# Optimization experiments

Measured on AMD Instinct MI355X. Metric: run time of the kernel, lower is better.

The kernel has to match this reference:

```python
import jax, jax.numpy as jnp
import numpy as np

D_MODEL = 1024
N_HEADS = 16
HEAD_DIM = D_MODEL // N_HEADS
D_FF = 4096
B, T = 2, 2048


def layernorm(x, g, b, eps=1e-5):
    mu = jnp.mean(x, axis=-1, keepdims=True)
    var = jnp.var(x, axis=-1, keepdims=True)
    return (x - mu) * jax.lax.rsqrt(var + eps) * g + b


def setup_inputs() -> dict:
    key = jax.random.key(0)
    ks = jax.random.split(key, 8)
    s = 0.02
    return {
        "x": jax.random.normal(ks[0], (B, T, D_MODEL), dtype=jnp.float32),
        "ln1_g": jnp.ones((D_MODEL,), jnp.float32),
        "ln1_b": jnp.zeros((D_MODEL,), jnp.float32),
        "qkv_w": jax.random.normal(ks[1], (D_MODEL, 3 * D_MODEL), jnp.float32) * s,
        "qkv_b": jnp.zeros((3 * D_MODEL,), jnp.float32),
        "proj_w": jax.random.normal(ks[2], (D_MODEL, D_MODEL), jnp.float32) * s,
        "proj_b": jnp.zeros((D_MODEL,), jnp.float32),
        "ln2_g": jnp.ones((D_MODEL,), jnp.float32),
        "ln2_b": jnp.zeros((D_MODEL,), jnp.float32),
        "mlp_w1": jax.random.normal(ks[3], (D_MODEL, D_FF), jnp.float32) * s,
        "mlp_b1": jnp.zeros((D_FF,), jnp.float32),
        "mlp_w2": jax.random.normal(ks[4], (D_FF, D_MODEL), jnp.float32) * s,
        "mlp_b2": jnp.zeros((D_MODEL,), jnp.float32),
    }


def reference(x, ln1_g, ln1_b, qkv_w, qkv_b, proj_w, proj_b,
              ln2_g, ln2_b, mlp_w1, mlp_b1, mlp_w2, mlp_b2):
    Bv, Tv, C = x.shape
    scale = HEAD_DIM ** -0.5
    # --- attention branch ---
    h = layernorm(x, ln1_g, ln1_b)
    qkv = h @ qkv_w + qkv_b                                   # [B,T,3C]
    qkv = qkv.reshape(Bv, Tv, 3, N_HEADS, HEAD_DIM)
    q, k, v = qkv[:, :, 0], qkv[:, :, 1], qkv[:, :, 2]        # [B,T,H,Dh]
    att = jnp.einsum('bqhd,bkhd->bhqk', q, k) * scale         # [B,H,T,T]
    causal = jnp.tril(jnp.ones((Tv, Tv), dtype=bool))
    att = jnp.where(causal[None, None], att, -jnp.inf)
    att = jax.nn.softmax(att, axis=-1)
    out = jnp.einsum('bhqk,bkhd->bqhd', att, v).reshape(Bv, Tv, C)
    out = out @ proj_w + proj_b
    x = x + out
    # --- mlp branch ---
    h2 = layernorm(x, ln2_g, ln2_b)
    h2 = jax.nn.gelu(h2 @ mlp_w1 + mlp_b1, approximate=False)
    x = x + (h2 @ mlp_w2 + mlp_b2)
    return x
```

## Files before the change

kernel.cpp:

```cpp
#include <hip/hip_runtime.h>
#include <hip/hip_bf16.h>
#include <cstdint>

typedef __attribute__((ext_vector_type(4))) float f32x4;
typedef __attribute__((ext_vector_type(16))) float f32x16;
typedef __attribute__((ext_vector_type(8))) __bf16 bf16x8;
typedef __attribute__((ext_vector_type(4))) __bf16 bf16x4;
typedef __attribute__((ext_vector_type(4))) uint32_t u32x4;
typedef __attribute__((ext_vector_type(2))) unsigned int u32x2;

#define EPI_BF16 0
#define EPI_GELU 1
#define EPI_RES  2

__device__ __forceinline__ void gll16(const void* g, void* l) {
  __builtin_amdgcn_global_load_lds((__attribute__((address_space(1))) void*)(g),
                                   (__attribute__((address_space(3))) void*)(l), 16, 0, 0);
}

__global__ __launch_bounds__(256)
void convT(const float* __restrict__ W, __bf16* __restrict__ WT, int Kd, int Nd)
{
  __shared__ __bf16 t[64][72];
  const int tid = threadIdx.x;
  const int n0 = blockIdx.x * 64, k0 = blockIdx.y * 64;
#pragma unroll
  for (int i = 0; i < 4; ++i) {
    const int c = i * 256 + tid;
    const int r = c >> 4, cc = (c & 15) * 4;
    const float4 v = *(const float4*)(W + (size_t)(k0 + r) * Nd + n0 + cc);
    bf16x4 tv; tv[0] = (__bf16)v.x; tv[1] = (__bf16)v.y; tv[2] = (__bf16)v.z; tv[3] = (__bf16)v.w;
    *(bf16x4*)&t[r][cc] = tv;
  }
  __syncthreads();
#pragma unroll
  for (int i = 0; i < 2; ++i) {
    const int c = i * 256 + tid;
    const int n = c >> 3, s = (c & 7) * 8;
    bf16x8 o;
#pragma unroll
    for (int j = 0; j < 8; ++j) o[j] = t[s + j][n];
    *(bf16x8*)(WT + (size_t)(n0 + n) * Kd + k0 + s) = o;
  }
}

__global__ __launch_bounds__(256)
void ln_rows(const float* __restrict__ x, const float* __restrict__ g,
             const float* __restrict__ b, __bf16* __restrict__ out)
{
  const int row = blockIdx.x;
  const int tid = threadIdx.x;
  const float4 v = *(const float4*)(x + (size_t)row * 1024 + tid * 4);
  float s = v.x + v.y + v.z + v.w;
  float q = v.x * v.x + v.y * v.y + v.z * v.z + v.w * v.w;
#pragma unroll
  for (int o = 32; o; o >>= 1) { s += __shfl_xor(s, o); q += __shfl_xor(q, o); }
  __shared__ float red[8];
  const int wid = tid >> 6;
  if ((tid & 63) == 0) { red[wid] = s; red[4 + wid] = q; }
  __syncthreads();
  s = red[0] + red[1] + red[2] + red[3];
  q = red[4] + red[5] + red[6] + red[7];
  const float mu = s * (1.0f / 1024.0f);
  const float var = q * (1.0f / 1024.0f) - mu * mu;
  const float rs = rsqrtf(var + 1e-5f);
  bf16x4 o4;
#pragma unroll
  for (int i = 0; i < 4; ++i) {
    const int c = tid * 4 + i;
    const float xv = (&v.x)[i];
    o4[i] = (__bf16)((xv - mu) * rs * g[c] + b[c]);
  }
  *(bf16x4*)(out + (size_t)row * 1024 + tid * 4) = o4;
}

template<int EPI>
__global__ __launch_bounds__(256)
void gemm_bt(const __bf16* __restrict__ A, const __bf16* __restrict__ BT,
             const float* __restrict__ bias, const float* __restrict__ R,
             void* __restrict__ Out, int M, int N, int K)
{
  const int tid = threadIdx.x;
  const int lane = tid & 63, wid = tid >> 6;
  const int l15 = lane & 15, lg = lane >> 4;
  const int wm = (wid >> 1) * 64, wn = (wid & 1) * 64;
  const int rowBase = blockIdx.y * 128, colBase = blockIdx.x * 128;
  __shared__ __bf16 As[128 * 32];
  __shared__ __bf16 Bs[128 * 32];
  f32x4 acc[4][4] = {};

  for (int k0 = 0; k0 < K; k0 += 32) {
#pragma unroll
    for (int i = 0; i < 2; ++i) {
      const int c = i * 256 + tid;
      const int r = c >> 2, s = (c & 3) * 8;
      gll16(A + (size_t)(rowBase + r) * K + (k0 + s), As + c * 8);
    }
#pragma unroll
    for (int i = 0; i < 2; ++i) {
      const int c = i * 256 + tid;
      const int r = c >> 2, s = (c & 3) * 8;
      gll16(BT + (size_t)(colBase + r) * K + (k0 + s), Bs + c * 8);
    }
    __syncthreads();
    bf16x8 af[4], bfr[4];
#pragma unroll
    for (int m = 0; m < 4; ++m) af[m] = *(const bf16x8*)(As + (wm + m * 16 + l15) * 32 + lg * 8);
#pragma unroll
    for (int n = 0; n < 4; ++n) bfr[n] = *(const bf16x8*)(Bs + (wn + n * 16 + l15) * 32 + lg * 8);
#pragma unroll
    for (int m = 0; m < 4; ++m)
#pragma unroll
      for (int n = 0; n < 4; ++n)
        acc[m][n] = __builtin_amdgcn_mfma_f32_16x16x32_bf16(af[m], bfr[n], acc[m][n], 0, 0, 0);
    __syncthreads();
  }
#pragma unroll
  for (int m = 0; m < 4; ++m) {
#pragma unroll
    for (int n = 0; n < 4; ++n) {
      const int col = colBase + wn + n * 16 + l15;
      const float bb = bias[col];
#pragma unroll
      for (int i = 0; i < 4; ++i) {
        const int row = rowBase + wm + m * 16 + lg * 4 + i;
        float v = acc[m][n][i] + bb;
        if constexpr (EPI == EPI_GELU) {
          v = 0.5f * v * (1.0f + erff(v * 0.70710678118654752f));
          ((__bf16*)Out)[(size_t)row * N + col] = (__bf16)v;
        } else if constexpr (EPI == EPI_BF16) {
          ((__bf16*)Out)[(size_t)row * N + col] = (__bf16)v;
        } else {
          v += R[(size_t)row * N + col];
          ((float*)Out)[(size_t)row * N + col] = v;
        }
      }
    }
  }
}

__global__ __launch_bounds__(256)
void rearrange(const __bf16* __restrict__ qkv, __bf16* __restrict__ Q,
               __bf16* __restrict__ Kb, __bf16* __restrict__ VT)
{
  __shared__ __bf16 vt[64][72];
  const int tid = threadIdx.x;
  const int bid = blockIdx.x;
  const int bh = bid >> 5, tt = bid & 31;
  const int b = bh >> 4, h = bh & 15;
  const int t0 = tt * 64;
#pragma unroll
  for (int i = 0; i < 2; ++i) {
    const int c = i * 256 + tid;
    const int tk = c >> 3, d0 = (c & 7) * 8;
    const size_t srow = (size_t)(b * 2048 + t0 + tk) * 3072 + h * 64 + d0;
    const size_t drow = (size_t)(bh * 2048 + t0 + tk) * 64 + d0;
    *(bf16x8*)(Q + drow) = *(const bf16x8*)(qkv + srow);
    *(bf16x8*)(Kb + drow) = *(const bf16x8*)(qkv + srow + 1024);
    *(bf16x8*)&vt[tk][d0] = *(const bf16x8*)(qkv + srow + 2048);
  }
  __syncthreads();
#pragma unroll
  for (int i = 0; i < 2; ++i) {
    const int c = i * 256 + tid;
    const int d = c >> 3, s = (c & 7) * 8;
    bf16x8 o;
#pragma unroll
    for (int j = 0; j < 8; ++j) o[j] = vt[s + j][d];
    *(bf16x8*)(VT + (size_t)(bh * 64 + d) * 2048 + t0 + s) = o;
  }
}

__global__ __launch_bounds__(128)
void attn(const __bf16* __restrict__ Q, const __bf16* __restrict__ K,
          const __bf16* __restrict__ VT, __bf16* __restrict__ O)
{
  const int bid = blockIdx.x;
  const int bh = bid >> 5, qt = 31 - (bid & 31);
  const int tid = threadIdx.x;
  const int lane = tid & 63, w = tid >> 6;
  const int l31 = lane & 31, hi = lane >> 5;
  __shared__ __bf16 Ks[64 * 64];
  __shared__ __bf16 Vs[64 * 64];
  const size_t base = (size_t)bh * 2048 * 64;
  const int qrow0 = qt * 64 + w * 32;
  const int xsw = (l31 & 7) << 3;

  bf16x8 qf[4];
#pragma unroll
  for (int s = 0; s < 4; ++s)
    qf[s] = *(const bf16x8*)(Q + base + (size_t)(qrow0 + l31) * 64 + s * 16 + hi * 8);

  f32x16 oa0 = {}, oa1 = {};
  float mst = -INFINITY, lst = 0.0f;

  for (int j = 0; j <= qt; ++j) {
#pragma unroll
    for (int rnd = 0; rnd < 4; ++rnd) {
      const int c = rnd * 128 + tid;
      const int r = c >> 3;
      const int e = ((c & 7) ^ (r & 7)) * 8;
      gll16(K + base + (size_t)(j * 64 + r) * 64 + e, Ks + c * 8);
      gll16(VT + base + (size_t)r * 2048 + j * 64 + e, Vs + c * 8);
    }
    __syncthreads();

    f32x16 s0v = {}, s1v = {};
#pragma unroll
    for (int s = 0; s < 4; ++s) {
      const int co = (s * 16 + hi * 8) ^ xsw;
      bf16x8 ak0 = *(const bf16x8*)(Ks + l31 * 64 + co);
      bf16x8 ak1 = *(const bf16x8*)(Ks + (32 + l31) * 64 + co);
      s0v = __builtin_amdgcn_mfma_f32_32x32x16_bf16(ak0, qf[s], s0v, 0, 0, 0);
      s1v = __builtin_amdgcn_mfma_f32_32x32x16_bf16(ak1, qf[s], s1v, 0, 0, 0);
    }
#pragma unroll
    for (int rg = 0; rg < 16; ++rg) { s0v[rg] *= 0.125f; s1v[rg] *= 0.125f; }
    if (j == qt) {
      const int qg = qrow0 + l31;
#pragma unroll
      for (int rg = 0; rg < 16; ++rg) {
        const int kr = j * 64 + ((rg & 3) + 8 * (rg >> 2)) + 4 * hi;
        if (kr > qg) s0v[rg] = -INFINITY;
        if (kr + 32 > qg) s1v[rg] = -INFINITY;
      }
    }
    float mx = s0v[0];
#pragma unroll
    for (int rg = 1; rg < 16; ++rg) mx = fmaxf(mx, s0v[rg]);
#pragma unroll
    for (int rg = 0; rg < 16; ++rg) mx = fmaxf(mx, s1v[rg]);
    mx = fmaxf(mx, __shfl_xor(mx, 32));
    const float mnew = fmaxf(mst, mx);
    const float cf = __expf(mst - mnew);
    float rs = 0.0f;
#pragma unroll
    for (int rg = 0; rg < 16; ++rg) {
      s0v[rg] = __expf(s0v[rg] - mnew); rs += s0v[rg];
      s1v[rg] = __expf(s1v[rg] - mnew); rs += s1v[rg];
    }
    rs += __shfl_xor(rs, 32);
    lst = lst * cf + rs;
    mst = mnew;
#pragma unroll
    for (int rg = 0; rg < 16; ++rg) {
      const float cb = __shfl(cf, (rg & 3) + 8 * (rg >> 2) + 4 * hi);
      oa0[rg] *= cb; oa1[rg] *= cb;
    }
#pragma unroll
    for (int s = 0; s < 4; ++s) {
      const int br = (s & 1) * 8;
      uint32_t wA0, wA1, wB0, wB1;
      if (s < 2) {
        asm("v_cvt_pk_bf16_f32 %0, %1, %2" : "=v"(wA0) : "v"(s0v[br + 0]), "v"(s0v[br + 1]));
        asm("v_cvt_pk_bf16_f32 %0, %1, %2" : "=v"(wA1) : "v"(s0v[br + 2]), "v"(s0v[br + 3]));
        asm("v_cvt_pk_bf16_f32 %0, %1, %2" : "=v"(wB0) : "v"(s0v[br + 4]), "v"(s0v[br + 5]));
        asm("v_cvt_pk_bf16_f32 %0, %1, %2" : "=v"(wB1) : "v"(s0v[br + 6]), "v"(s0v[br + 7]));
      } else {
        asm("v_cvt_pk_bf16_f32 %0, %1, %2" : "=v"(wA0) : "v"(s1v[br + 0]), "v"(s1v[br + 1]));
        asm("v_cvt_pk_bf16_f32 %0, %1, %2" : "=v"(wA1) : "v"(s1v[br + 2]), "v"(s1v[br + 3]));
        asm("v_cvt_pk_bf16_f32 %0, %1, %2" : "=v"(wB0) : "v"(s1v[br + 4]), "v"(s1v[br + 5]));
        asm("v_cvt_pk_bf16_f32 %0, %1, %2" : "=v"(wB1) : "v"(s1v[br + 6]), "v"(s1v[br + 7]));
      }
      const u32x2 r0 = __builtin_amdgcn_permlane32_swap(wA0, wB0, false, false);
      const u32x2 r1 = __builtin_amdgcn_permlane32_swap(wA1, wB1, false, false);
      u32x4 uu; uu.x = r0.x; uu.y = r1.x; uu.z = r0.y; uu.w = r1.y;
      const bf16x8 pa = __builtin_bit_cast(bf16x8, uu);
      const int co = (s * 16 + hi * 8) ^ xsw;
      bf16x8 bv0 = *(const bf16x8*)(Vs + l31 * 64 + co);
      bf16x8 bv1 = *(const bf16x8*)(Vs + (32 + l31) * 64 + co);
      oa0 = __builtin_amdgcn_mfma_f32_32x32x16_bf16(pa, bv0, oa0, 0, 0, 0);
      oa1 = __builtin_amdgcn_mfma_f32_32x32x16_bf16(pa, bv1, oa1, 0, 0, 0);
    }
    __syncthreads();
  }
  const float inv = 1.0f / lst;
  const int b = bh >> 4, hd = bh & 15;
#pragma unroll
  for (int rg = 0; rg < 16; ++rg) {
    const int cr = (rg & 3) + 8 * (rg >> 2) + 4 * hi;
    const float ib = __shfl(inv, cr);
    const int qr = qrow0 + cr;
    O[(size_t)(b * 2048 + qr) * 1024 + hd * 64 + l31]      = (__bf16)(oa0[rg] * ib);
    O[(size_t)(b * 2048 + qr) * 1024 + hd * 64 + 32 + l31] = (__bf16)(oa1[rg] * ib);
  }
}

extern "C" void kernel_launch(void* const* d_in, const int* in_sizes, int n_in,
                              void* d_out, int out_size, void* d_ws, size_t ws_size,
                              hipStream_t stream)
{
  const float* x      = (const float*)d_in[0];
  const float* ln1_g  = (const float*)d_in[1];
  const float* ln1_b  = (const float*)d_in[2];
  const float* qkv_w  = (const float*)d_in[3];
  const float* qkv_b  = (const float*)d_in[4];
  const float* proj_w = (const float*)d_in[5];
  const float* proj_b = (const float*)d_in[6];
  const float* ln2_g  = (const float*)d_in[7];
  const float* ln2_b  = (const float*)d_in[8];
  const float* mlp_w1 = (const float*)d_in[9];
  const float* mlp_b1 = (const float*)d_in[10];
  const float* mlp_w2 = (const float*)d_in[11];
  const float* mlp_b2 = (const float*)d_in[12];

  char* ws = (char*)d_ws;
  __bf16* qkvT  = (__bf16*)(ws + 0);
  __bf16* projT = (__bf16*)(ws + 6291456);
  __bf16* w1T   = (__bf16*)(ws + 8388608);
  __bf16* w2T   = (__bf16*)(ws + 16777216);
  __bf16* h1    = (__bf16*)(ws + 25165824);
  __bf16* qkv   = (__bf16*)(ws + 33554432);
  __bf16* act1  = (__bf16*)(ws + 33554432);
  __bf16* Qb    = (__bf16*)(ws + 58720256);
  __bf16* Kb    = (__bf16*)(ws + 67108864);
  __bf16* VTb   = (__bf16*)(ws + 75497472);
  __bf16* attO  = (__bf16*)(ws + 83886080);
  float*  x2    = (float*) (ws + 92274688);
  __bf16* h2    = (__bf16*)(ws + 109051904);

  convT<<<dim3(48, 16), 256, 0, stream>>>(qkv_w, qkvT, 1024, 3072);
  convT<<<dim3(16, 16), 256, 0, stream>>>(proj_w, projT, 1024, 1024);
  convT<<<dim3(64, 16), 256, 0, stream>>>(mlp_w1, w1T, 1024, 4096);
  convT<<<dim3(16, 64), 256, 0, stream>>>(mlp_w2, w2T, 4096, 1024);

  ln_rows<<<4096, 256, 0, stream>>>(x, ln1_g, ln1_b, h1);
  gemm_bt<EPI_BF16><<<dim3(24, 32), 256, 0, stream>>>(h1, qkvT, qkv_b, nullptr, qkv, 4096, 3072, 1024);
  rearrange<<<1024, 256, 0, stream>>>(qkv, Qb, Kb, VTb);
  attn<<<1024, 128, 0, stream>>>(Qb, Kb, VTb, attO);
  gemm_bt<EPI_RES><<<dim3(8, 32), 256, 0, stream>>>(attO, projT, proj_b, x, x2, 4096, 1024, 1024);
  ln_rows<<<4096, 256, 0, stream>>>(x2, ln2_g, ln2_b, h2);
  gemm_bt<EPI_GELU><<<dim3(32, 32), 256, 0, stream>>>(h2, w1T, mlp_b1, nullptr, act1, 4096, 4096, 1024);
  gemm_bt<EPI_RES><<<dim3(8, 32), 256, 0, stream>>>(act1, w2T, mlp_b2, x2, (float*)d_out, 4096, 1024, 4096);
}
```

Baseline: 443.6 us.

## Swizzle GEMM LDS layout, remap workgroups across XCDs, split-K the final MLP GEMM

```diff
diff --git a/kernel.cpp b/kernel.cpp
--- a/kernel.cpp
+++ b/kernel.cpp
@@ -12,6 +12,7 @@
 #define EPI_BF16 0
 #define EPI_GELU 1
 #define EPI_RES  2
+#define EPI_PART 3
 
 __device__ __forceinline__ void gll16(const void* g, void* l) {
   __builtin_amdgcn_global_load_lds((__attribute__((address_space(1))) void*)(g),
@@ -84,30 +85,39 @@
   const int lane = tid & 63, wid = tid >> 6;
   const int l15 = lane & 15, lg = lane >> 4;
   const int wm = (wid >> 1) * 64, wn = (wid & 1) * 64;
-  const int rowBase = blockIdx.y * 128, colBase = blockIdx.x * 128;
+  const int nwg = gridDim.x * gridDim.y;
+  const int hw = blockIdx.y * gridDim.x + blockIdx.x;
+  const int logical = (hw & 7) * (nwg >> 3) + (hw >> 3);
+  const int rowBase = (logical / gridDim.x) * 128;
+  const int colBase = (logical % gridDim.x) * 128;
+  const int kLen = K / gridDim.z;
+  const int kBeg = blockIdx.z * kLen;
   __shared__ __bf16 As[128 * 32];
   __shared__ __bf16 Bs[128 * 32];
   f32x4 acc[4][4] = {};
-
-  for (int k0 = 0; k0 < K; k0 += 32) {
+  const int fsw = ((l15 >> 1) & 3) << 3;
+
+  for (int k0 = kBeg; k0 < kBeg + kLen; k0 += 32) {
 #pragma unroll
     for (int i = 0; i < 2; ++i) {
       const int c = i * 256 + tid;
-      const int r = c >> 2, s = (c & 3) * 8;
+      const int r = c >> 2;
+      const int s = ((c & 3) ^ ((r >> 1) & 3)) * 8;
       gll16(A + (size_t)(rowBase + r) * K + (k0 + s), As + c * 8);
     }
 #pragma unroll
     for (int i = 0; i < 2; ++i) {
       const int c = i * 256 + tid;
-      const int r = c >> 2, s = (c & 3) * 8;
+      const int r = c >> 2;
+      const int s = ((c & 3) ^ ((r >> 1) & 3)) * 8;
       gll16(BT + (size_t)(colBase + r) * K + (k0 + s), Bs + c * 8);
     }
     __syncthreads();
     bf16x8 af[4], bfr[4];
 #pragma unroll
-    for (int m = 0; m < 4; ++m) af[m] = *(const bf16x8*)(As + (wm + m * 16 + l15) * 32 + lg * 8);
-#pragma unroll
-    for (int n = 0; n < 4; ++n) bfr[n] = *(const bf16x8*)(Bs + (wn + n * 16 + l15) * 32 + lg * 8);
+    for (int m = 0; m < 4; ++m) af[m] = *(const bf16x8*)(As + (wm + m * 16 + l15) * 32 + (lg * 8 ^ fsw));
+#pragma unroll
+    for (int n = 0; n < 4; ++n) bfr[n] = *(const bf16x8*)(Bs + (wn + n * 16 + l15) * 32 + (lg * 8 ^ fsw));
 #pragma unroll
     for (int m = 0; m < 4; ++m)
 #pragma unroll
@@ -120,7 +130,8 @@
 #pragma unroll
     for (int n = 0; n < 4; ++n) {
       const int col = colBase + wn + n * 16 + l15;
-      const float bb = bias[col];
+      float bb = 0.0f;
+      if constexpr (EPI != EPI_PART) bb = bias[col];
 #pragma unroll
       for (int i = 0; i < 4; ++i) {
         const int row = rowBase + wm + m * 16 + lg * 4 + i;
@@ -130,13 +141,32 @@
           ((__bf16*)Out)[(size_t)row * N + col] = (__bf16)v;
         } else if constexpr (EPI == EPI_BF16) {
           ((__bf16*)Out)[(size_t)row * N + col] = (__bf16)v;
-        } else {
+        } else if constexpr (EPI == EPI_RES) {
           v += R[(size_t)row * N + col];
           ((float*)Out)[(size_t)row * N + col] = v;
+        } else {
+          ((float*)Out)[((size_t)blockIdx.z * M + row) * N + col] = v;
         }
       }
     }
   }
+}
+
+__global__ __launch_bounds__(256)
+void reduce2(const float* __restrict__ P, const float* __restrict__ bias,
+             const float* __restrict__ R, float* __restrict__ Out, int MN, int N)
+{
+  const size_t e = ((size_t)blockIdx.x * 256 + threadIdx.x) * 4;
+  const float4 a = *(const float4*)(P + e);
+  const float4 b = *(const float4*)(P + (size_t)MN + e);
+  const float4 r = *(const float4*)(R + e);
+  const float4 bb = *(const float4*)(bias + (e & (size_t)(N - 1)));
+  float4 o;
+  o.x = a.x + b.x + r.x + bb.x;
+  o.y = a.y + b.y + r.y + bb.y;
+  o.z = a.z + b.z + r.z + bb.z;
+  o.w = a.w + b.w + r.w + bb.w;
+  *(float4*)(Out + e) = o;
 }
 
 __global__ __launch_bounds__(256)
@@ -309,15 +339,16 @@
   __bf16* projT = (__bf16*)(ws + 6291456);
   __bf16* w1T   = (__bf16*)(ws + 8388608);
   __bf16* w2T   = (__bf16*)(ws + 16777216);
-  __bf16* h1    = (__bf16*)(ws + 25165824);
-  __bf16* qkv   = (__bf16*)(ws + 33554432);
-  __bf16* act1  = (__bf16*)(ws + 33554432);
-  __bf16* Qb    = (__bf16*)(ws + 58720256);
-  __bf16* Kb    = (__bf16*)(ws + 67108864);
-  __bf16* VTb   = (__bf16*)(ws + 75497472);
-  __bf16* attO  = (__bf16*)(ws + 83886080);
-  float*  x2    = (float*) (ws + 92274688);
-  __bf16* h2    = (__bf16*)(ws + 109051904);
+  float*  x2    = (float*) (ws + 25165824);
+  __bf16* act1  = (__bf16*)(ws + 41943040);
+  __bf16* h1    = (__bf16*)(ws + 41943040);
+  __bf16* qkv   = (__bf16*)(ws + 50331648);
+  float*  part  = (float*) (ws + 75497472);
+  __bf16* h2    = (__bf16*)(ws + 75497472);
+  __bf16* Qb    = (__bf16*)(ws + 75497472);
+  __bf16* Kb    = (__bf16*)(ws + 83886080);
+  __bf16* VTb   = (__bf16*)(ws + 92274688);
+  __bf16* attO  = (__bf16*)(ws + 100663296);
 
   convT<<<dim3(48, 16), 256, 0, stream>>>(qkv_w, qkvT, 1024, 3072);
   convT<<<dim3(16, 16), 256, 0, stream>>>(proj_w, projT, 1024, 1024);
@@ -331,5 +362,6 @@
   gemm_bt<EPI_RES><<<dim3(8, 32), 256, 0, stream>>>(attO, projT, proj_b, x, x2, 4096, 1024, 1024);
   ln_rows<<<4096, 256, 0, stream>>>(x2, ln2_g, ln2_b, h2);
   gemm_bt<EPI_GELU><<<dim3(32, 32), 256, 0, stream>>>(h2, w1T, mlp_b1, nullptr, act1, 4096, 4096, 1024);
-  gemm_bt<EPI_RES><<<dim3(8, 32), 256, 0, stream>>>(act1, w2T, mlp_b2, x2, (float*)d_out, 4096, 1024, 4096);
-}
+  gemm_bt<EPI_PART><<<dim3(8, 32, 2), 256, 0, stream>>>(act1, w2T, nullptr, nullptr, part, 4096, 1024, 4096);
+  reduce2<<<4096, 256, 0, stream>>>(part, mlp_b2, x2, (float*)d_out, 4096 * 1024, 1024);
+}
```

Measured after the change: 417.6 us. -5.8%, faster.
